# Kernel optimization log

Hardware: AMD Instinct MI355X
Metric: run time of the kernel (lower is better)

## Reference

```python
import jax, jax.numpy as jnp
import numpy as np

N = 50000        # nodes
E = 800000       # edges
F_IN = 32        # float features (x also carries 1 trailing cell-id column)
CELL_DIM = 16
NUM_CELLS = 854
C = 64           # out_channels
H0, H1 = 2, 1    # heads schedule for num_layers=2 -> [2, 1]
D_IN = F_IN + CELL_DIM  # 48, GAT input dim after cell embedding concat
NEG_SLOPE = 0.2  # PyG GATConv default negative_slope


def setup_inputs() -> dict:
    key = jax.random.key(0)
    ks = jax.random.split(key, 14)
    base = jax.random.normal(ks[0], (N, F_IN), jnp.float32)
    cell_ids = jax.random.randint(ks[1], (N,), 0, NUM_CELLS)
    x = jnp.concatenate([base, cell_ids.astype(jnp.float32)[:, None]], axis=1)
    edge_index = jax.random.randint(ks[2], (2, E), 0, N, dtype=jnp.int32)
    s = lambda f: 1.0 / np.sqrt(f)
    emb = jax.random.normal(ks[3], (NUM_CELLS, CELL_DIM), jnp.float32)
    W0 = jax.random.normal(ks[4], (D_IN, H0 * C), jnp.float32) * s(D_IN)
    a_src0 = jax.random.normal(ks[5], (H0, C), jnp.float32) * s(C)
    a_dst0 = jax.random.normal(ks[6], (H0, C), jnp.float32) * s(C)
    b0 = jnp.zeros((C,), jnp.float32)
    ln_g = jnp.ones((C,), jnp.float32)
    ln_b = jnp.zeros((C,), jnp.float32)
    W1 = jax.random.normal(ks[7], (C, H1 * C), jnp.float32) * s(C)
    a_src1 = jax.random.normal(ks[8], (H1, C), jnp.float32) * s(C)
    a_dst1 = jax.random.normal(ks[9], (H1, C), jnp.float32) * s(C)
    b1 = jnp.zeros((C,), jnp.float32)
    return {"x": x, "edge_index": edge_index, "emb": emb,
            "W0": W0, "a_src0": a_src0, "a_dst0": a_dst0, "b0": b0,
            "ln_g": ln_g, "ln_b": ln_b,
            "W1": W1, "a_src1": a_src1, "a_dst1": a_dst1, "b1": b1}


def gat_layer(h_in, src, dst, W, a_src, a_dst, b, heads):
    # h_in: [N, D]; src/dst: [E'] (self-loops already appended)
    h = (h_in @ W).reshape(N, heads, C)                 # [N, H, C]
    alpha_s = jnp.einsum('nhc,hc->nh', h, a_src)        # [N, H]
    alpha_d = jnp.einsum('nhc,hc->nh', h, a_dst)
    e = jax.nn.leaky_relu(alpha_s[src] + alpha_d[dst], NEG_SLOPE)  # [E', H]
    # segment softmax over incoming edges of each dst node
    m = jax.ops.segment_max(e, dst, num_segments=N)     # [N, H]
    ex = jnp.exp(e - m[dst])
    denom = jax.ops.segment_sum(ex, dst, num_segments=N)
    alpha = ex / denom[dst]                             # [E', H]
    msg = h[src] * alpha[:, :, None]                    # [E', H, C]
    out = jax.ops.segment_sum(msg, dst, num_segments=N) # [N, H, C]
    return out.mean(axis=1) + b                         # concat=False -> mean over heads


def layer_norm(x, g, b):
    mu = x.mean(-1, keepdims=True)
    var = ((x - mu) ** 2).mean(-1, keepdims=True)
    return (x - mu) * jax.lax.rsqrt(var + 1e-5) * g + b


def reference(x, edge_index, emb, W0, a_src0, a_dst0, b0, ln_g, ln_b,
              W1, a_src1, a_dst1, b1):
    base = x[:, :-1]
    cell_ids = x[:, -1].astype(jnp.int32)
    h = jnp.concatenate([base, emb[cell_ids]], axis=1)  # [N, 48]
    # add self-loops (PyG GATConv default add_self_loops=True)
    loop = jnp.arange(N, dtype=edge_index.dtype)
    src = jnp.concatenate([edge_index[0], loop])
    dst = jnp.concatenate([edge_index[1], loop])
    h = gat_layer(h, src, dst, W0, a_src0, a_dst0, b0, H0)
    h = jax.nn.elu(layer_norm(h, ln_g, ln_b))           # dropout is identity at eval
    h = gat_layer(h, src, dst, W1, a_src1, a_dst1, b1, H1)
    return h
```

## Files before the change

### kernel.cpp

```cpp
#include <hip/hip_runtime.h>
#include <hip/hip_bf16.h>

#define N_NODES 50000
#define N_EDGES 800000
#define E_TOT 850000
#define F_IN 32
#define CELL_DIM 16
#define D_IN 48
#define X_STRIDE 33
#define NUM_CELLS 854
#define NEG_SLOPE 0.2f
#define SCAN_BLOCKS 49
#define NODE0_BLOCKS 2048
#define HIST_BLOCKS 3125

typedef unsigned int uint;
typedef unsigned short ushort;

static __device__ __forceinline__ uint f2b(float f) {
  uint x = __float_as_uint(f);
  return (x + 0x7fffu + ((x >> 16) & 1u)) >> 16;
}
static __device__ __forceinline__ float b2f_lo(uint w) { return __uint_as_float(w << 16); }
static __device__ __forceinline__ float b2f_hi(uint w) { return __uint_as_float(w & 0xffff0000u); }
static __device__ __forceinline__ float lrelu(float e) { return e > 0.f ? e : NEG_SLOPE * e; }


__global__ __launch_bounds__(256) void k_node0h(const float* __restrict__ x,
                                                const float* __restrict__ emb,
                                                const float* __restrict__ W0,
                                                const float* __restrict__ asrc,
                                                const float* __restrict__ adst,
                                                const int* __restrict__ ei,
                                                ushort* __restrict__ h0u,
                                                float* __restrict__ as0, float* __restrict__ ad0,
                                                int* __restrict__ deg) {
  int tid = threadIdx.x;
  if (blockIdx.x >= NODE0_BLOCKS) {
    int e = (blockIdx.x - NODE0_BLOCKS) * 256 + tid;
    if (e < N_EDGES) atomicAdd(&deg[ei[N_EDGES + e]], 1);
    return;
  }
  __shared__ float hin[8][48];
  int lane = tid & 63, wid = tid >> 6;
  int h = wid & 1;
  int q = wid >> 1;
  float w0r[D_IN];
#pragma unroll
  for (int k = 0; k < D_IN; ++k) w0r[k] = W0[k * 128 + h * 64 + lane];
  float av_s = asrc[h * 64 + lane], av_d = adst[h * 64 + lane];

  for (int g = blockIdx.x; g < N_NODES / 8; g += NODE0_BLOCKS) {
    int nb = g * 8;
#pragma unroll
    for (int j = 0; j < 2; ++j) {
      int loc = 2 * wid + j;
      int n = nb + loc;
      float t = 0.f;
      if (lane < 33) t = x[n * X_STRIDE + lane];
      int cid = (int)__shfl(t, 32, 64);
      cid = cid < 0 ? 0 : (cid >= NUM_CELLS ? NUM_CELLS - 1 : cid);
      if (lane >= 32 && lane < 48) t = emb[cid * CELL_DIM + (lane - 32)];
      if (lane < 48) hin[loc][lane] = t;
    }
    __syncthreads();
#pragma unroll
    for (int j = 0; j < 4; ++j) {
      int loc = 4 * q + j;
      int n = nb + loc;
      const float4* hp = (const float4*)hin[loc];
      float acc = 0.f;
#pragma unroll
      for (int k4 = 0; k4 < 12; ++k4) {
        float4 hh = hp[k4];
        acc = fmaf(hh.x, w0r[4 * k4 + 0], acc);
        acc = fmaf(hh.y, w0r[4 * k4 + 1], acc);
        acc = fmaf(hh.z, w0r[4 * k4 + 2], acc);
        acc = fmaf(hh.w, w0r[4 * k4 + 3], acc);
      }
      h0u[(n * 64 + lane) * 2 + h] = (ushort)f2b(acc);
      float sa = acc * av_s, sd = acc * av_d;
#pragma unroll
      for (int o = 32; o >= 1; o >>= 1) {
        sa += __shfl_xor(sa, o, 64);
        sd += __shfl_xor(sd, o, 64);
      }
      if (lane == 0) {
        as0[n * 2 + h] = sa;
        ad0[n * 2 + h] = sd;
      }
    }
    __syncthreads();
  }
}


__global__ __launch_bounds__(1024) void k_scan1(const int* __restrict__ deg, int* __restrict__ off,
                                                int* __restrict__ bsum) {
  __shared__ int ws[16];
  int tid = threadIdx.x;
  int lane = tid & 63, wid = tid >> 6;
  int i = blockIdx.x * 1024 + tid;
  int v = (i < N_NODES) ? deg[i] + 1 : 0;
  int sc = v;
#pragma unroll
  for (int o = 1; o < 64; o <<= 1) {
    int t = __shfl_up(sc, o, 64);
    if (lane >= o) sc += t;
  }
  if (lane == 63) ws[wid] = sc;
  __syncthreads();
  if (tid < 16) {
    int w = ws[tid];
    int s = w;
#pragma unroll
    for (int o = 1; o < 16; o <<= 1) {
      int t = __shfl_up(s, o, 64);
      if (tid >= o) s += t;
    }
    ws[tid] = s - w;
  }
  __syncthreads();
  int excl = sc - v + ws[wid];
  if (i < N_NODES) off[i] = excl;
  if (tid == 1023) bsum[blockIdx.x] = excl + v;
}

__global__ __launch_bounds__(1024) void k_scan23(int* __restrict__ off, int* __restrict__ ofs,
                                                 const int* __restrict__ bsum) {
  __shared__ int carry_s;
  int tid = threadIdx.x;
  if (tid < 64) {
    int v = (tid < SCAN_BLOCKS) ? bsum[tid] : 0;
    int s = v;
#pragma unroll
    for (int o = 1; o < 64; o <<= 1) {
      int t = __shfl_up(s, o, 64);
      if (tid >= o) s += t;
    }
    if (tid == (int)blockIdx.x) carry_s = s - v;
  }
  __syncthreads();
  int carry = carry_s;
  int i = blockIdx.x * 1024 + tid;
  if (i < N_NODES) {
    int v = off[i] + carry;
    off[i] = v;
    ofs[i] = v;
  }
  if (i == 0) off[N_NODES] = E_TOT;
}

__global__ __launch_bounds__(256) void k_scatter(const int* __restrict__ ei, int* __restrict__ ofs,
                                                 const int* __restrict__ off,
                                                 const float2* __restrict__ as0v,
                                                 const float2* __restrict__ ad0v,
                                                 uint2* __restrict__ ew) {
  int t = blockIdx.x * 256 + threadIdx.x;
  if (t < N_EDGES) {
    int s = ei[t], d = ei[N_EDGES + t];
    float2 a_s = as0v[s], a_d = ad0v[d];
    float w0 = __expf(lrelu(a_s.x + a_d.x));
    float w1 = __expf(lrelu(a_s.y + a_d.y));
    int p = atomicAdd(&ofs[d], 1);
    ew[p] = make_uint2((uint)s, f2b(w0) | (f2b(w1) << 16));
  } else if (t < N_EDGES + N_NODES) {
    int n = t - N_EDGES;
    int slot = off[n + 1] - 1;
    float2 a_s = as0v[n], a_d = ad0v[n];
    float w0 = __expf(lrelu(a_s.x + a_d.x));
    float w1 = __expf(lrelu(a_s.y + a_d.y));
    ew[slot] = make_uint2((uint)n, f2b(w0) | (f2b(w1) << 16));
  }
}


__global__ __launch_bounds__(256) void k_agg0(const int* __restrict__ off,
                                              const uint2* __restrict__ ew,
                                              const uint* __restrict__ h0p,
                                              const float* __restrict__ b0,
                                              const float* __restrict__ lng,
                                              const float* __restrict__ lnb,
                                              const float* __restrict__ W1,
                                              const float* __restrict__ asrc1,
                                              const float* __restrict__ adst1,
                                              ushort* __restrict__ h1b,
                                              float* __restrict__ as1, float* __restrict__ ad1) {
  __shared__ float yb[4][64];
  int n = blockIdx.x * 4 + (threadIdx.x >> 6);
  int lane = threadIdx.x & 63;
  int wl = threadIdx.x >> 6;
  float acc0 = 0.f, acc1 = 0.f, den0 = 0.f, den1 = 0.f;
  int i0 = off[n], i1 = off[n + 1];
  int nbt = (i1 - i0 + 7) >> 3;
  for (int b = 0; b < nbt; ++b) {
    int base = i0 + b * 8;
    uint2 r[8];
    uint h[8];
#pragma unroll
    for (int j = 0; j < 8; ++j) r[j] = ew[base + j];
#pragma unroll
    for (int j = 0; j < 8; ++j) {
      uint sx = (base + j < i1) ? r[j].x : 0u;
      h[j] = h0p[sx * 64 + lane];
    }
#pragma unroll
    for (int j = 0; j < 8; ++j) {
      uint wy = (base + j < i1) ? r[j].y : 0u;
      float w;
      w = b2f_lo(wy); acc0 += w * b2f_lo(h[j]); den0 += w;
      w = b2f_hi(wy); acc1 += w * b2f_hi(h[j]); den1 += w;
    }
  }
  float v = 0.5f * (acc0 / den0 + acc1 / den1) + b0[lane];
  float mu = v;
#pragma unroll
  for (int o = 32; o >= 1; o >>= 1) mu += __shfl_xor(mu, o, 64);
  mu *= (1.0f / 64.0f);
  float d = v - mu;
  float vr = d * d;
#pragma unroll
  for (int o = 32; o >= 1; o >>= 1) vr += __shfl_xor(vr, o, 64);
  vr *= (1.0f / 64.0f);
  float y = d * rsqrtf(vr + 1e-5f) * lng[lane] + lnb[lane];
  y = y > 0.f ? y : expm1f(y);
  yb[wl][lane] = y;
  const float4* yp = (const float4*)yb[wl];
  float p0 = 0.f, p1 = 0.f, p2 = 0.f, p3 = 0.f;
#pragma unroll
  for (int k4 = 0; k4 < 16; ++k4) {
    float4 yy = yp[k4];
    p0 = fmaf(yy.x, W1[(4 * k4 + 0) * 64 + lane], p0);
    p1 = fmaf(yy.y, W1[(4 * k4 + 1) * 64 + lane], p1);
    p2 = fmaf(yy.z, W1[(4 * k4 + 2) * 64 + lane], p2);
    p3 = fmaf(yy.w, W1[(4 * k4 + 3) * 64 + lane], p3);
  }
  float h1v = (p0 + p1) + (p2 + p3);
  h1b[n * 64 + lane] = (ushort)f2b(h1v);
  float sa = h1v * asrc1[lane];
  float sdv = h1v * adst1[lane];
#pragma unroll
  for (int o = 32; o >= 1; o >>= 1) {
    sa += __shfl_xor(sa, o, 64);
    sdv += __shfl_xor(sdv, o, 64);
  }
  if (lane == 0) {
    as1[n] = sa;
    ad1[n] = sdv;
  }
}


__global__ __launch_bounds__(256) void k_agg1(const int* __restrict__ off,
                                              const uint2* __restrict__ ew,
                                              const ushort* __restrict__ h1b,
                                              const float* __restrict__ as1,
                                              const float* __restrict__ ad1,
                                              const float* __restrict__ b1,
                                              float* __restrict__ out) {
  int n = blockIdx.x * 4 + (threadIdx.x >> 6);
  int lane = threadIdx.x & 63;
  float adv = ad1[n];
  float acc = 0.f, den = 0.f;
  int i0 = off[n], i1 = off[n + 1];
  int nbt = (i1 - i0 + 7) >> 3;
  for (int b = 0; b < nbt; ++b) {
    int base = i0 + b * 8;
    uint s[8];
    float a[8];
    uint h[8];
#pragma unroll
    for (int j = 0; j < 8; ++j) {
      uint sx = ew[base + j].x;
      s[j] = (base + j < i1) ? sx : 0u;
    }
#pragma unroll
    for (int j = 0; j < 8; ++j) a[j] = as1[s[j]];
#pragma unroll
    for (int j = 0; j < 8; ++j) h[j] = h1b[s[j] * 64 + lane];
#pragma unroll
    for (int j = 0; j < 8; ++j) {
      float w = __expf(lrelu(a[j] + adv));
      w = (base + j < i1) ? w : 0.f;
      acc += w * __uint_as_float(h[j] << 16);
      den += w;
    }
  }
  out[n * 64 + lane] = acc / den + b1[lane];
}


extern "C" void kernel_launch(void* const* d_in, const int* in_sizes, int n_in,
                              void* d_out, int out_size, void* d_ws, size_t ws_size,
                              hipStream_t stream) {
  const float* x    = (const float*)d_in[0];
  const int*   ei   = (const int*)d_in[1];
  const float* emb  = (const float*)d_in[2];
  const float* W0   = (const float*)d_in[3];
  const float* as0w = (const float*)d_in[4];
  const float* ad0w = (const float*)d_in[5];
  const float* b0   = (const float*)d_in[6];
  const float* lng  = (const float*)d_in[7];
  const float* lnb  = (const float*)d_in[8];
  const float* W1   = (const float*)d_in[9];
  const float* as1w = (const float*)d_in[10];
  const float* ad1w = (const float*)d_in[11];
  const float* b1   = (const float*)d_in[12];
  float* out = (float*)d_out;

  uint2* ew  = (uint2*)d_ws;
  float* as0 = (float*)(ew + E_TOT);
  float* ad0 = as0 + N_NODES * 2;
  float* as1 = ad0 + N_NODES * 2;
  float* ad1 = as1 + N_NODES;
  uint* h0p = (uint*)(ad1 + N_NODES);
  ushort* h1b = (ushort*)(h0p + N_NODES * 64);
  int* deg  = (int*)(h1b + N_NODES * 64);
  int* off  = deg + N_NODES;
  int* ofs  = off + N_NODES + 1;
  int* bsum = ofs + N_NODES;

  hipMemsetAsync(deg, 0, N_NODES * sizeof(int), stream);
  k_node0h<<<NODE0_BLOCKS + HIST_BLOCKS, 256, 0, stream>>>(x, emb, W0, as0w, ad0w, ei,
                                                           (ushort*)h0p, as0, ad0, deg);
  k_scan1<<<SCAN_BLOCKS, 1024, 0, stream>>>(deg, off, bsum);
  k_scan23<<<SCAN_BLOCKS, 1024, 0, stream>>>(off, ofs, bsum);
  k_scatter<<<(N_EDGES + N_NODES + 255) / 256, 256, 0, stream>>>(ei, ofs, off, (const float2*)as0,
                                                                 (const float2*)ad0, ew);
  k_agg0<<<N_NODES / 4, 256, 0, stream>>>(off, ew, h0p, b0, lng, lnb, W1, as1w, ad1w,
                                          h1b, as1, ad1);
  k_agg1<<<N_NODES / 4, 256, 0, stream>>>(off, ew, h1b, as1, ad1, b1, out);
}
```

Measured before the change: 268.4 us.

## Gather neighbor rows via global_load_lds with lane-cooperative edge record loads

Both aggregation kernels now process incoming edges in windows of 24. One coalesced load per lane fetches the edge records, and readlane broadcasts them as scalars. Neighbor feature rows are gathered with direct global-to-LDS loads, with a vmcnt wait before the accumulate loop. In layer 1, the attention weights are computed once per lane instead of redundantly by all lanes. The aim is more gathers in flight and fewer redundant loads, at the cost of 24KB of extra LDS per block, which can lower occupancy, and a full wait per window.

```diff
diff --git a/kernel.cpp b/kernel.cpp
--- a/kernel.cpp
+++ b/kernel.cpp
@@ -13,6 +13,7 @@
 #define SCAN_BLOCKS 49
 #define NODE0_BLOCKS 2048
 #define HIST_BLOCKS 3125
+#define W 24
 
 typedef unsigned int uint;
 typedef unsigned short ushort;
@@ -186,32 +187,36 @@
                                               const float* __restrict__ adst1,
                                               ushort* __restrict__ h1b,
                                               float* __restrict__ as1, float* __restrict__ ad1) {
+  __shared__ uint gbuf[4][W * 64];
   __shared__ float yb[4][64];
-  int n = blockIdx.x * 4 + (threadIdx.x >> 6);
-  int lane = threadIdx.x & 63;
-  int wl = threadIdx.x >> 6;
+  int tid = threadIdx.x;
+  int lane = tid & 63, wl = tid >> 6;
+  int n = blockIdx.x * 4 + wl;
+  int i0 = off[n], i1 = off[n + 1];
   float acc0 = 0.f, acc1 = 0.f, den0 = 0.f, den1 = 0.f;
-  int i0 = off[n], i1 = off[n + 1];
-  int nbt = (i1 - i0 + 7) >> 3;
-  for (int b = 0; b < nbt; ++b) {
-    int base = i0 + b * 8;
-    uint2 r[8];
-    uint h[8];
-#pragma unroll
-    for (int j = 0; j < 8; ++j) r[j] = ew[base + j];
-#pragma unroll
-    for (int j = 0; j < 8; ++j) {
-      uint sx = (base + j < i1) ? r[j].x : 0u;
-      h[j] = h0p[sx * 64 + lane];
-    }
-#pragma unroll
-    for (int j = 0; j < 8; ++j) {
-      uint wy = (base + j < i1) ? r[j].y : 0u;
+  uint* gb = gbuf[wl];
+
+  for (int w0 = i0; w0 < i1; w0 += W) {
+    uint2 rec = make_uint2(0u, 0u);
+    if (lane < W && w0 + lane < i1) rec = ew[w0 + lane];
+#pragma unroll
+    for (int j = 0; j < W; ++j) {
+      uint sx = (uint)__builtin_amdgcn_readlane((int)rec.x, j);
+      __builtin_amdgcn_global_load_lds((const uint*)(h0p + sx * 64u + (uint)lane),
+                                       gb + j * 64, 4, 0, 0);
+    }
+    asm volatile("s_waitcnt vmcnt(0)" ::: "memory");
+    __builtin_amdgcn_sched_barrier(0);
+#pragma unroll
+    for (int j = 0; j < W; ++j) {
+      uint wy = (uint)__builtin_amdgcn_readlane((int)rec.y, j);
+      uint h = gb[j * 64 + lane];
       float w;
-      w = b2f_lo(wy); acc0 += w * b2f_lo(h[j]); den0 += w;
-      w = b2f_hi(wy); acc1 += w * b2f_hi(h[j]); den1 += w;
-    }
-  }
+      w = b2f_lo(wy); acc0 += w * b2f_lo(h); den0 += w;
+      w = b2f_hi(wy); acc1 += w * b2f_hi(h); den1 += w;
+    }
+  }
+
   float v = 0.5f * (acc0 / den0 + acc1 / den1) + b0[lane];
   float mu = v;
 #pragma unroll
@@ -258,32 +263,38 @@
                                               const float* __restrict__ ad1,
                                               const float* __restrict__ b1,
                                               float* __restrict__ out) {
-  int n = blockIdx.x * 4 + (threadIdx.x >> 6);
-  int lane = threadIdx.x & 63;
+  __shared__ uint gbuf[4][W * 64];
+  int tid = threadIdx.x;
+  int lane = tid & 63, wl = tid >> 6;
+  int n = blockIdx.x * 4 + wl;
+  int i0 = off[n], i1 = off[n + 1];
   float adv = ad1[n];
   float acc = 0.f, den = 0.f;
-  int i0 = off[n], i1 = off[n + 1];
-  int nbt = (i1 - i0 + 7) >> 3;
-  for (int b = 0; b < nbt; ++b) {
-    int base = i0 + b * 8;
-    uint s[8];
-    float a[8];
-    uint h[8];
-#pragma unroll
-    for (int j = 0; j < 8; ++j) {
-      uint sx = ew[base + j].x;
-      s[j] = (base + j < i1) ? sx : 0u;
-    }
-#pragma unroll
-    for (int j = 0; j < 8; ++j) a[j] = as1[s[j]];
-#pragma unroll
-    for (int j = 0; j < 8; ++j) h[j] = h1b[s[j] * 64 + lane];
-#pragma unroll
-    for (int j = 0; j < 8; ++j) {
-      float w = __expf(lrelu(a[j] + adv));
-      w = (base + j < i1) ? w : 0.f;
-      acc += w * __uint_as_float(h[j] << 16);
-      den += w;
+  uint* gb = gbuf[wl];
+  const ushort* gbs = (const ushort*)gb;
+
+  for (int w0 = i0; w0 < i1; w0 += W) {
+    bool val = (lane < W) && (w0 + lane < i1);
+    uint rx = 0u;
+    if (val) rx = ew[w0 + lane].x;
+    float av = val ? as1[rx] : 0.f;
+    float wlane = val ? __expf(lrelu(av + adv)) : 0.f;
+    uint hl = lane & 31;
+#pragma unroll
+    for (int j = 0; j < W; ++j) {
+      uint sx = (uint)__builtin_amdgcn_readlane((int)rx, j);
+      __builtin_amdgcn_global_load_lds((const uint*)(h1b + sx * 64u) + hl,
+                                       gb + j * 64, 4, 0, 0);
+    }
+    asm volatile("s_waitcnt vmcnt(0)" ::: "memory");
+    __builtin_amdgcn_sched_barrier(0);
+#pragma unroll
+    for (int j = 0; j < W; ++j) {
+      float wj = __uint_as_float((uint)__builtin_amdgcn_readlane(
+          (int)__float_as_uint(wlane), j));
+      uint hh = (uint)gbs[j * 128 + lane];
+      acc = fmaf(wj, __uint_as_float(hh << 16), acc);
+      den += wj;
     }
   }
   out[n * 64 + lane] = acc / den + b1[lane];
```

New measurement: 270.8 us. About the same (+0.9%).
